# Optimization experiments

Hardware: AMD Instinct MI355X
Metric: run time of the kernel (lower is better)

## Reference

```python
import jax, jax.numpy as jnp
import numpy as np

B, S, DIN, DIM = 4, 4096, 256, 256
GAMMA = 0.9865


def setup_inputs() -> dict:
    key = jax.random.key(0)
    ks = jax.random.split(key, 9)
    inp = {
        'xq': jax.random.normal(ks[0], (B, S, DIN), dtype=jnp.float32),
        'xk': jax.random.normal(ks[1], (B, S, DIN), dtype=jnp.float32),
        'xv': jax.random.normal(ks[2], (B, S, DIN), dtype=jnp.float32),
        'Wq': jax.random.normal(ks[3], (DIN, DIM), dtype=jnp.float32) * 0.05,
        'bq': jnp.zeros((DIM,), dtype=jnp.float32),
        'Wk': jax.random.normal(ks[4], (DIN, DIM), dtype=jnp.float32) * 0.05,
        'bk': jnp.zeros((DIM,), dtype=jnp.float32),
        'Wv': jax.random.normal(ks[5], (DIN, DIM), dtype=jnp.float32) * 0.05,
        'bv': jnp.zeros((DIM,), dtype=jnp.float32),
    }
    return inp


def _decay_matrix(s, gamma):
    # D[i, j] = gamma^(i-j) if i >= j else 0
    idx = jnp.arange(s)
    diff = idx[:, None] - idx[None, :]
    D = jnp.where(diff >= 0,
                  jnp.power(jnp.float32(gamma), diff.astype(jnp.float32)),
                  jnp.float32(0.0))
    return D


def reference(xq, xk, xv, Wq, bq, Wk, bk, Wv, bv):
    Q = xq @ Wq + bq  # [B,S,D]
    K = xk @ Wk + bk  # [B,S,D]
    V = xv @ Wv + bv  # [B,S,D]
    d = Q.shape[-1]
    # scores[b,i,j] = Q[b,i] . K[b,j] / sqrt(d)
    x = jnp.einsum('bid,bjd->bij', Q, K) / jnp.sqrt(jnp.float32(d))
    D = _decay_matrix(S, GAMMA)
    # Faithful to TF broadcasting: divides along the LAST axis (per-column by
    # sqrt of that index's row-sum): D[i,j] /= sqrt(sum_k D[j,k])
    D = D / jnp.sqrt(jnp.sum(D, axis=-1))
    x = x * D  # broadcast [B,S,S] * [S,S]
    # _norm_3 per batch element with TF broadcasting: x[b,i,j] /= max(|sum_k x[b,j,k]|, 1)
    denom = jnp.maximum(jnp.abs(jnp.sum(x, axis=-1)), 1.0)  # [B,S]
    x = x / denom[:, None, :]
    return x @ V  # [B,S,D]
```

## Files before the change

### kernel.cpp

```cpp
#include <hip/hip_runtime.h>
#include <math.h>

#define BB 4
#define SS 4096
#define DD 256
#define LL 256
#define NCH 16
#define GAMMA 0.9865f
#define LOG2G (-0.019609034f)
#define INV1MG 74.07407407f
#define SLAB 1032
#define SLABB 520

typedef __attribute__((ext_vector_type(8))) short short8;
typedef __attribute__((ext_vector_type(4))) float f32x4;
typedef unsigned short u16;
typedef unsigned int u32;

__device__ __forceinline__ u16 f2bf(float f) {
  union { float f; unsigned u; } v; v.f = f;
  unsigned r = v.u + 0x7FFFu + ((v.u >> 16) & 1u);
  return (u16)(r >> 16);
}
__device__ __forceinline__ float bf2f(u16 h) {
  union { unsigned u; float f; } v; v.u = ((unsigned)h) << 16; return v.f;
}

__device__ __forceinline__ void gll16(const u16* g, u16* l) {
  __builtin_amdgcn_global_load_lds(
      (const __attribute__((address_space(1))) u32*)g,
      (__attribute__((address_space(3))) u32*)l, 16, 0, 0);
}
__device__ __forceinline__ void stage8kp(const u16* g, u16* l, int lane) {
#pragma unroll
  for (int i = 0; i < 8; ++i)
    gll16(g + i * 512 + lane * 8, l + (i >> 1) * SLAB + (i & 1) * 512);
}
__device__ __forceinline__ void stageB64(const u16* g, u16* l, int lane) {
#pragma unroll
  for (int i = 0; i < 4; ++i)
    gll16(g + i * 1024 + lane * 8, l + i * SLABB);
}
__device__ __forceinline__ void stageAB(
    const u16* AhP, const u16* AlP, const u16* BhP, const u16* BlP, int ks,
    u16* Ab, u16* Bb, int wave, int lane)
{
  if (wave == 0) stage8kp(AhP + ks * 4096, Ab, lane);
  if (wave == 1) stage8kp(AlP + ks * 4096, Ab + 4 * SLAB, lane);
  if (wave == 2) stageB64(BhP + ks * 4096, Bb, lane);
  if (wave == 3) stageB64(BlP + ks * 4096, Bb + 4 * SLABB, lane);
}

__device__ __forceinline__ void mfma_step_slab(
    const u16* Ah, const u16* Al, const u16* Bh, const u16* Bl,
    int wm0, int wn0, int fm, int fq, f32x4 acc[4][4])
{
  const int ka = fq * SLAB;
  short8 ah[4], al[4];
#pragma unroll
  for (int i = 0; i < 4; ++i) {
    ah[i] = *(const short8*)&Ah[ka + (wm0 + i * 16 + fm) * 8];
    al[i] = *(const short8*)&Al[ka + (wm0 + i * 16 + fm) * 8];
  }
#pragma unroll
  for (int j = 0; j < 4; ++j) {
    short8 bh = *(const short8*)&Bh[ka + (wn0 + j * 16 + fm) * 8];
    short8 bl = *(const short8*)&Bl[ka + (wn0 + j * 16 + fm) * 8];
#pragma unroll
    for (int i = 0; i < 4; ++i) {
      acc[i][j] = __builtin_amdgcn_mfma_f32_16x16x32_bf16(al[i], bh, acc[i][j], 0, 0, 0);
      acc[i][j] = __builtin_amdgcn_mfma_f32_16x16x32_bf16(ah[i], bl, acc[i][j], 0, 0, 0);
      acc[i][j] = __builtin_amdgcn_mfma_f32_16x16x32_bf16(ah[i], bh, acc[i][j], 0, 0, 0);
    }
  }
}

__device__ __forceinline__ void mfma_step_ab(
    const u16* Ah, const u16* Al, const u16* Bh, const u16* Bl,
    int wm0, int wn0, int fm, int fq, f32x4 acc[4][2])
{
  const int ka = fq * SLAB, kb = fq * SLABB;
  short8 ah[4], al[4];
#pragma unroll
  for (int i = 0; i < 4; ++i) {
    ah[i] = *(const short8*)&Ah[ka + (wm0 + i * 16 + fm) * 8];
    al[i] = *(const short8*)&Al[ka + (wm0 + i * 16 + fm) * 8];
  }
#pragma unroll
  for (int j = 0; j < 2; ++j) {
    short8 bh = *(const short8*)&Bh[kb + (wn0 + j * 16 + fm) * 8];
    short8 bl = *(const short8*)&Bl[kb + (wn0 + j * 16 + fm) * 8];
#pragma unroll
    for (int i = 0; i < 4; ++i) {
      acc[i][j] = __builtin_amdgcn_mfma_f32_16x16x32_bf16(al[i], bh, acc[i][j], 0, 0, 0);
      acc[i][j] = __builtin_amdgcn_mfma_f32_16x16x32_bf16(ah[i], bl, acc[i][j], 0, 0, 0);
      acc[i][j] = __builtin_amdgcn_mfma_f32_16x16x32_bf16(ah[i], bh, acc[i][j], 0, 0, 0);
    }
  }
}

__device__ __forceinline__ void bounce_write(
    float* fb, const f32x4 acc[4][4], int wm0, int wn0, int fm, int fq, int p)
{
  if (wn0 == p * 64) {
#pragma unroll
    for (int i = 0; i < 4; ++i)
#pragma unroll
      for (int j = 0; j < 4; ++j)
#pragma unroll
        for (int r = 0; r < 4; ++r)
          fb[(wm0 + i * 16 + fq * 4 + r) * 65 + j * 16 + fm] = acc[i][j][r];
  }
}

__global__ __launch_bounds__(256) void init_pack_kernel(
    const float* __restrict__ Wq, const float* __restrict__ Wk, const float* __restrict__ Wv,
    u16* __restrict__ Wth, u16* __restrict__ Wtl,
    float* __restrict__ rsP, float* __restrict__ lVec)
{
  const int which = blockIdx.x;
  const int it = blockIdx.y;
  const int t = threadIdx.x;
  if (which == 0) {
    *(float4*)&rsP[(size_t)(it * 256 + t) * 4] = (float4){0.f, 0.f, 0.f, 0.f};
  } else if (which == 1) {
    *(float4*)&lVec[(size_t)(it * 256 + t) * 4] = (float4){0.f, 0.f, 0.f, 0.f};
  }
  const float* W = which == 0 ? Wq : (which == 1 ? Wk : Wv);
  for (int pn = 0; pn < 2; ++pn) {
    int pos = it * 256 + t;
    int k8 = pos >> 7, r = pos & 127;
    u16 hs[8], ls[8];
#pragma unroll
    for (int u = 0; u < 8; ++u) {
      float x = W[(size_t)(k8 * 8 + u) * DD + pn * 128 + r];
      u16 h = f2bf(x); hs[u] = h; ls[u] = f2bf(x - bf2f(h));
    }
    size_t o = ((size_t)((which * 2 + pn) * 32 + k8)) * 1024 + (size_t)r * 8;
    *(short8*)&Wth[o] = *(short8*)hs;
    *(short8*)&Wtl[o] = *(short8*)ls;
  }
}

__device__ __forceinline__ void loadX(float xs[2][8], const float* XP, int ks,
                                      int arow, int ak8) {
#pragma unroll
  for (int t = 0; t < 2; ++t) {
    const float* src = XP + (size_t)(t * 64 + arow) * DD + ks * 32 + ak8 * 8;
    *(float4*)&xs[t][0] = *(const float4*)src;
    *(float4*)&xs[t][4] = *(const float4*)(src + 4);
  }
}
__device__ __forceinline__ void writeAsplit(u16* Ab, const float xs[2][8],
                                            int arow, int ak8) {
#pragma unroll
  for (int t = 0; t < 2; ++t) {
    int row = t * 64 + arow;
    u16 hs[8], ls[8];
#pragma unroll
    for (int u = 0; u < 8; ++u) {
      u16 h = f2bf(xs[t][u]); hs[u] = h; ls[u] = f2bf(xs[t][u] - bf2f(h));
    }
    *(short8*)&Ab[ak8 * SLAB + row * 8] = *(short8*)hs;
    *(short8*)&Ab[4 * SLAB + ak8 * SLAB + row * 8] = *(short8*)ls;
  }
}

__global__ __launch_bounds__(256, 2) void proj_kernel(
    const float* __restrict__ xq, const float* __restrict__ xk, const float* __restrict__ xv,
    const u16* __restrict__ Wth, const u16* __restrict__ Wtl,
    const float* __restrict__ bq, const float* __restrict__ bk_, const float* __restrict__ bv,
    u16* __restrict__ Qh, u16* __restrict__ Ql,
    u16* __restrict__ Kh, u16* __restrict__ Kl,
    u16* __restrict__ KTh, u16* __restrict__ KTl, float* __restrict__ VT32,
    float* __restrict__ lVec)
{
  const int which = blockIdx.z;
  const float* bias = which == 0 ? bq : (which == 1 ? bk_ : bv);
  const int m0 = blockIdx.x * 128;
  const int pn = blockIdx.y;
  __shared__ u16 SM[2 * 16 * SLAB];
  __shared__ float rsc[128];
  __shared__ float wlut[128];
  __shared__ float kacc[64];
  float* fb = (float*)SM;
  const int tid = threadIdx.x, lane = tid & 63, wave = tid >> 6;
  const int wm0 = (wave >> 1) * 64, wn0 = (wave & 1) * 64;
  const int fm = lane & 15, fq = lane >> 4;
  if (which == 1) {
    if (tid < 128) {
      int sb = (m0 & (SS - 1)) + tid;
      rsc[tid] = rsqrtf((1.0f - exp2f((float)(sb + 1) * LOG2G)) * INV1MG);
      wlut[tid] = exp2f((float)(255 - ((m0 & (LL - 1)) + tid)) * LOG2G);
    }
    if (tid < 64) kacc[tid] = 0.f;
  }
  const float* XP = (which == 0 ? xq : (which == 1 ? xk : xv)) + (size_t)m0 * DD;
  const u16* WhP = Wth + (size_t)((which * 2 + pn) * 32) * 1024;
  const u16* WlP = Wtl + (size_t)((which * 2 + pn) * 32) * 1024;
  const int arow = tid >> 2, ak8 = tid & 3;
  f32x4 acc[4][4];
#pragma unroll
  for (int i = 0; i < 4; ++i)
#pragma unroll
    for (int j = 0; j < 4; ++j) acc[i][j] = (f32x4){0.f, 0.f, 0.f, 0.f};
  float xs[2][8];
  loadX(xs, XP, 0, arow, ak8);
  writeAsplit(SM, xs, arow, ak8);
  if (wave == 2) stage8kp(WhP, SM + 8 * SLAB, lane);
  if (wave == 3) stage8kp(WlP, SM + 12 * SLAB, lane);
  int cur = 0;
  for (int ks = 0; ks < 8; ++ks) {
    __syncthreads();
    u16* Bc = cur ? SM + 16 * SLAB : SM;
    u16* Bn = cur ? SM : SM + 16 * SLAB;
    if (ks < 7) {
      loadX(xs, XP, ks + 1, arow, ak8);
      if (wave == 2) stage8kp(WhP + (ks + 1) * 4096, Bn + 8 * SLAB, lane);
      if (wave == 3) stage8kp(WlP + (ks + 1) * 4096, Bn + 12 * SLAB, lane);
    }
    mfma_step_slab(Bc, Bc + 4 * SLAB, Bc + 8 * SLAB, Bc + 12 * SLAB,
                   wm0, wn0, fm, fq, acc);
    if (ks < 7) writeAsplit(Bn, xs, arow, ak8);
    cur ^= 1;
  }
  const int b = m0 >> 12, sbb = m0 & (SS - 1);
  for (int p = 0; p < 2; ++p) {
    __syncthreads();
    bounce_write(fb, acc, wm0, wn0, fm, fq, p);
    __syncthreads();
    if (which == 0) {
#pragma unroll
      for (int it = 0; it < 4; ++it) {
        int unit = it * 256 + tid;
        int k8l = unit >> 7, row = unit & 127;
        int gcol0 = pn * 128 + p * 64 + k8l * 8;
        u16 hs[8], ls[8];
#pragma unroll
        for (int u = 0; u < 8; ++u) {
          float v = (fb[row * 65 + k8l * 8 + u] + bias[gcol0 + u]) * (1.f / 16.f);
          u16 h = f2bf(v); hs[u] = h; ls[u] = f2bf(v - bf2f(h));
        }
        size_t o = (size_t)(m0 >> 7) * 32768 + (size_t)(pn * 16 + p * 8 + k8l) * 1024 + row * 8;
        *(short8*)&Qh[o] = *(short8*)hs;
        *(short8*)&Ql[o] = *(short8*)ls;
      }
    } else if (which == 1) {
#pragma unroll
      for (int it = 0; it < 4; ++it) {
        int unit = it * 256 + tid;
        int k8l = unit >> 7, row = unit & 127;
        int gcol0 = pn * 128 + p * 64 + k8l * 8;
        u16 hs[8], ls[8];
#pragma unroll
        for (int u = 0; u < 8; ++u) {
          float v = (fb[row * 65 + k8l * 8 + u] + bias[gcol0 + u]) * rsc[row];
          u16 h = f2bf(v); hs[u] = h; ls[u] = f2bf(v - bf2f(h));
        }
        size_t o = (size_t)(m0 >> 7) * 32768 + (size_t)(pn * 16 + p * 8 + k8l) * 1024 + row * 8;
        *(short8*)&Kh[o] = *(short8*)hs;
        *(short8*)&Kl[o] = *(short8*)ls;
      }
      float kpart = 0.f;
#pragma unroll
      for (int it = 0; it < 4; ++it) {
        int unit = it * 256 + tid;
        int dl = unit & 63, s8l = unit >> 6;
        int gcolg = pn * 128 + p * 64 + dl;
        float bs = bias[gcolg];
        u16 hs[8], ls[8];
#pragma unroll
        for (int u = 0; u < 8; ++u) {
          int row = s8l * 8 + u;
          float v = (fb[row * 65 + dl] + bs) * rsc[row];
          kpart = fmaf(v, wlut[row], kpart);
          u16 h = f2bf(v); hs[u] = h; ls[u] = f2bf(v - bf2f(h));
        }
        int sb0 = sbb + s8l * 8;
        size_t o = ((size_t)(b * 2 + (gcolg >> 7)) * 512 + (sb0 >> 3)) * 1024 + (size_t)(gcolg & 127) * 8;
        *(short8*)&KTh[o] = *(short8*)hs;
        *(short8*)&KTl[o] = *(short8*)ls;
      }
      atomicAdd(&kacc[tid & 63], kpart);
      __syncthreads();
      if (tid < 64) {
        int c = sbb >> 8;
        atomicAdd(&lVec[(size_t)(b * NCH + c) * DD + pn * 128 + p * 64 + tid], kacc[tid]);
        kacc[tid] = 0.f;
      }
    } else {
#pragma unroll
      for (int it = 0; it < 4; ++it) {
        int unit = it * 256 + tid;
        int dl = unit & 63, s8l = unit >> 6;
        int gcolg = pn * 128 + p * 64 + dl;
        float bs = bias[gcolg];
        float vv[8];
#pragma unroll
        for (int u = 0; u < 8; ++u) vv[u] = fb[(s8l * 8 + u) * 65 + dl] + bs;
        float* dst = &VT32[(size_t)b * DD * SS + (size_t)gcolg * SS + sbb + s8l * 8];
        *(float4*)dst = (float4){vv[0], vv[1], vv[2], vv[3]};
        *(float4*)(dst + 4) = (float4){vv[4], vv[5], vv[6], vv[7]};
      }
    }
  }
}

__global__ __launch_bounds__(256, 3) void scores_kernel(
    const u16* __restrict__ Qh, const u16* __restrict__ Ql,
    const u16* __restrict__ Kh, const u16* __restrict__ Kl,
    const float* __restrict__ lVec, u16* __restrict__ Sgh, u16* __restrict__ Sgl,
    float* __restrict__ rsP)
{
  const int chunk = blockIdx.x, b = chunk >> 4, c = chunk & 15;
  const int y = blockIdx.y;
  const int m0 = (y < 2) ? 0 : 128;
  const int jn0 = (y < 2) ? y * 64 : (y - 2) * 64;
  __shared__ u16 SA[2 * 8 * SLAB];
  __shared__ u16 SB[2 * 8 * SLABB];
  __shared__ float cv[256], lut[256], rowAcc[128], qd2[2][128];
  float* fb = (float*)SA;
  const int tid = threadIdx.x, lane = tid & 63, wave = tid >> 6;
  const int wm0 = (wave >> 1) * 64, wn0 = (wave & 1) * 32;
  const int fm = lane & 15, fq = lane >> 4;
  if (jn0 == 0) {
    const float gL = exp2f((float)LL * LOG2G);
    float s = 0.f;
    for (int cp = 0; cp < c; ++cp)
      s = fmaf(gL, s, lVec[(size_t)(b * NCH + cp) * DD + tid]);
    cv[tid] = s;
  }
  lut[tid] = exp2f((float)tid * LOG2G);
  if (tid < 128) rowAcc[tid] = 0.f;
  const int growA = b * SS + c * LL + m0;
  const int growB = b * SS + c * LL + jn0;
  const u16* QhP = Qh + (size_t)(growA >> 7) * 32768;
  const u16* QlP = Ql + (size_t)(growA >> 7) * 32768;
  const u16* KhP = Kh + (size_t)(growB >> 7) * 32768 + (size_t)(growB & 127) * 8;
  const u16* KlP = Kl + (size_t)(growB >> 7) * 32768 + (size_t)(growB & 127) * 8;
  f32x4 acc[4][2];
#pragma unroll
  for (int i = 0; i < 4; ++i)
#pragma unroll
    for (int j = 0; j < 2; ++j) acc[i][j] = (f32x4){0.f, 0.f, 0.f, 0.f};
  float qdreg = 0.f;
  const int qrow = tid & 127, qk8b = tid >> 7;
  stageAB(QhP, QlP, KhP, KlP, 0, SA, SB, wave, lane);
  int cur = 0;
  for (int ks = 0; ks < 8; ++ks) {
    __syncthreads();
    u16* Ac = cur ? SA + 8 * SLAB : SA;
    u16* Bc = cur ? SB + 8 * SLABB : SB;
    u16* An = cur ? SA : SA + 8 * SLAB;
    u16* Bn = cur ? SB : SB + 8 * SLABB;
    if (ks < 7) stageAB(QhP, QlP, KhP, KlP, ks + 1, An, Bn, wave, lane);
    mfma_step_ab(Ac, Ac + 4 * SLAB, Bc, Bc + 4 * SLABB, wm0, wn0, fm, fq, acc);
    if (jn0 == 0) {
#pragma unroll
      for (int h2 = 0; h2 < 2; ++h2) {
        int k8l = qk8b + 2 * h2;
        const u16* ahp = &Ac[k8l * SLAB + qrow * 8];
        const u16* alp = &Ac[4 * SLAB + k8l * SLAB + qrow * 8];
#pragma unroll
        for (int u = 0; u < 8; ++u)
          qdreg = fmaf(bf2f(ahp[u]) + bf2f(alp[u]), cv[ks * 32 + k8l * 8 + u], qdreg);
      }
    }
    cur ^= 1;
  }
  qd2[qk8b][qrow] = qdreg;
  const int ps = chunk * 2 + (m0 >> 7);
  for (int rh = 0; rh < 2; ++rh) {
    __syncthreads();
    if (wm0 == rh * 64) {
#pragma unroll
      for (int i = 0; i < 4; ++i)
#pragma unroll
        for (int j = 0; j < 2; ++j)
#pragma unroll
          for (int r = 0; r < 4; ++r)
            fb[(i * 16 + fq * 4 + r) * 65 + wn0 + j * 16 + fm] = acc[i][j][r];
    }
    __syncthreads();
#pragma unroll
    for (int it = 0; it < 2; ++it) {
      int unit = it * 256 + tid;
      int k8l = unit >> 6, rowl = unit & 63;
      int il = m0 + rh * 64 + rowl;
      int jlb = jn0 + k8l * 8;
      float part = 0.f;
      u16 hs[8], ls[8];
#pragma unroll
      for (int u = 0; u < 8; ++u) {
        int jl = jlb + u;
        float v = (jl <= il) ? fb[rowl * 65 + k8l * 8 + u] * lut[il - jl] : 0.f;
        part += v;
        u16 h = f2bf(v); hs[u] = h; ls[u] = f2bf(v - bf2f(h));
      }
      atomicAdd(&rowAcc[rh * 64 + rowl], part);
      size_t o = (size_t)(ps * 32 + (jn0 >> 3) + k8l) * 1024 + (size_t)(rh * 64 + rowl) * 8;
      *(short8*)&Sgh[o] = *(short8*)hs;
      *(short8*)&Sgl[o] = *(short8*)ls;
    }
  }
  __syncthreads();
  if (tid < 128) {
    float rs = rowAcc[tid];
    if (jn0 == 0)
      rs += exp2f((float)(m0 + tid + 1) * LOG2G) * (qd2[0][tid] + qd2[1][tid]);
    atomicAdd(&rsP[(size_t)b * SS + c * LL + m0 + tid], rs);
  }
}

__global__ __launch_bounds__(256, 3) void lmat_kernel(
    const float* __restrict__ VT32, const float* __restrict__ rsP,
    const u16* __restrict__ KTh, const u16* __restrict__ KTl,
    float* __restrict__ lMatT)
{
  const int chunk = blockIdx.x, b = chunk >> 4, c = chunk & 15;
  const int ty = blockIdx.y;
  const int m0 = (ty >> 2) * 128, n0 = (ty & 3) * 64;
  __shared__ u16 SA[2 * 8 * SLAB];
  __shared__ u16 SB[2 * 8 * SLABB];
  __shared__ float swl[256];
  const int tid = threadIdx.x, lane = tid & 63, wave = tid >> 6;
  const int wm0 = (wave >> 1) * 64, wn0 = (wave & 1) * 32;
  const int fm = lane & 15, fq = lane >> 4;
  swl[tid] = exp2f((float)(255 - tid) * LOG2G) /
             fmaxf(fabsf(rsP[(size_t)b * SS + c * LL + tid]), 1.0f);
  const float* AP = VT32 + (size_t)b * DD * SS + (size_t)m0 * SS + c * LL;
  const u16* BhP = KTh + ((size_t)(b * 2 + (n0 >> 7)) * 512 + c * 32) * 1024 + (size_t)(n0 & 127) * 8;
  const u16* BlP = KTl + ((size_t)(b * 2 + (n0 >> 7)) * 512 + c * 32) * 1024 + (size_t)(n0 & 127) * 8;
  const int arow = tid >> 1;
  f32x4 acc[4][2];
#pragma unroll
  for (int i = 0; i < 4; ++i)
#pragma unroll
    for (int j = 0; j < 2; ++j) acc[i][j] = (f32x4){0.f, 0.f, 0.f, 0.f};
  float as[2][8];
#pragma unroll
  for (int t = 0; t < 2; ++t) {
    int ak8 = (tid & 1) * 2 + t;
    const float* src = AP + (size_t)arow * SS + ak8 * 8;
    *(float4*)&as[t][0] = *(const float4*)src;
    *(float4*)&as[t][4] = *(const float4*)(src + 4);
  }
  __syncthreads();
#pragma unroll
  for (int t = 0; t < 2; ++t) {
    int ak8 = (tid & 1) * 2 + t;
    u16 hs[8], ls[8];
#pragma unroll
    for (int u = 0; u < 8; ++u) {
      float v = as[t][u] * swl[ak8 * 8 + u];
      u16 h = f2bf(v); hs[u] = h; ls[u] = f2bf(v - bf2f(h));
    }
    *(short8*)&SA[ak8 * SLAB + arow * 8] = *(short8*)hs;
    *(short8*)&SA[4 * SLAB + ak8 * SLAB + arow * 8] = *(short8*)ls;
  }
  if (wave == 2) stageB64(BhP, SB, lane);
  if (wave == 3) stageB64(BlP, SB + 4 * SLABB, lane);
  int cur = 0;
  for (int ks = 0; ks < 8; ++ks) {
    __syncthreads();
    u16* Ac = cur ? SA + 8 * SLAB : SA;
    u16* Bc = cur ? SB + 8 * SLABB : SB;
    u16* An = cur ? SA : SA + 8 * SLAB;
    u16* Bn = cur ? SB : SB + 8 * SLABB;
    if (ks < 7) {
#pragma unroll
      for (int t = 0; t < 2; ++t) {
        int ak8 = (tid & 1) * 2 + t;
        const float* src = AP + (size_t)arow * SS + (ks + 1) * 32 + ak8 * 8;
        *(float4*)&as[t][0] = *(const float4*)src;
        *(float4*)&as[t][4] = *(const float4*)(src + 4);
      }
      if (wave == 2) stageB64(BhP + (ks + 1) * 4096, Bn, lane);
      if (wave == 3) stageB64(BlP + (ks + 1) * 4096, Bn + 4 * SLABB, lane);
    }
    mfma_step_ab(Ac, Ac + 4 * SLAB, Bc, Bc + 4 * SLABB, wm0, wn0, fm, fq, acc);
    if (ks < 7) {
#pragma unroll
      for (int t = 0; t < 2; ++t) {
        int ak8 = (tid & 1) * 2 + t;
        u16 hs[8], ls[8];
#pragma unroll
        for (int u = 0; u < 8; ++u) {
          float v = as[t][u] * swl[(ks + 1) * 32 + ak8 * 8 + u];
          u16 h = f2bf(v); hs[u] = h; ls[u] = f2bf(v - bf2f(h));
        }
        *(short8*)&An[ak8 * SLAB + arow * 8] = *(short8*)hs;
        *(short8*)&An[4 * SLAB + ak8 * SLAB + arow * 8] = *(short8*)ls;
      }
    }
    cur ^= 1;
  }
#pragma unroll
  for (int i = 0; i < 4; ++i)
#pragma unroll
    for (int j = 0; j < 2; ++j)
#pragma unroll
      for (int r = 0; r < 4; ++r) {
        int e = m0 + wm0 + i * 16 + fq * 4 + r;
        int d = n0 + wn0 + j * 16 + fm;
        lMatT[(size_t)chunk * 65536 + (size_t)e * 256 + d] = acc[i][j][r];
      }
}

__global__ __launch_bounds__(256) void combine_mat_kernel(
    const float* __restrict__ lMatT, u16* __restrict__ cMh, u16* __restrict__ cMl)
{
  const int t = blockIdx.x * 256 + threadIdx.x;
  const int b = t >> 13, rem = t & 8191;
  const int k8 = rem >> 8, e = rem & 255;
  const float gL = powf(GAMMA, (float)LL);
  float s[8] = {0.f, 0.f, 0.f, 0.f, 0.f, 0.f, 0.f, 0.f};
  for (int ch = 0; ch < 16; ++ch) {
    size_t ro = (size_t)(b * 16 + ch) * 65536 + (size_t)e * 256 + k8 * 8;
    float4 a0 = *(const float4*)&lMatT[ro];
    float4 a1 = *(const float4*)&lMatT[ro + 4];
    float vals[8] = {a0.x, a0.y, a0.z, a0.w, a1.x, a1.y, a1.z, a1.w};
    u16 hh[8], ll[8];
#pragma unroll
    for (int u = 0; u < 8; ++u) {
      u16 h = f2bf(s[u]); hh[u] = h; ll[u] = f2bf(s[u] - bf2f(h));
    }
    size_t wo = ((size_t)(((b * 16 + ch) * 2 + (e >> 7)) * 32 + k8)) * 1024 + (size_t)(e & 127) * 8;
    *(short8*)&cMh[wo] = *(short8*)hh;
    *(short8*)&cMl[wo] = *(short8*)ll;
#pragma unroll
    for (int u = 0; u < 8; ++u) s[u] = gL * s[u] + vals[u];
  }
}

__global__ __launch_bounds__(256, 3) void out_kernel(
    const u16* __restrict__ Qh, const u16* __restrict__ Ql,
    const u16* __restrict__ cMh, const u16* __restrict__ cMl,
    const u16* __restrict__ Sgh, const u16* __restrict__ Sgl,
    const float* __restrict__ VT32, const float* __restrict__ rsP,
    float* __restrict__ out)
{
  const int chunk = blockIdx.x, b = chunk >> 4, c = chunk & 15;
  const int ty = blockIdx.y;
  const int m0 = (ty >> 2) * 128, n0 = (ty & 3) * 64;
  __shared__ u16 SA[2 * 8 * SLAB];
  __shared__ u16 SB[2 * 8 * SLABB];
  __shared__ float olut[128];
  __shared__ float sdn[256];
  const int tid = threadIdx.x, lane = tid & 63, wave = tid >> 6;
  const int wm0 = (wave >> 1) * 64, wn0 = (wave & 1) * 32;
  const int fm = lane & 15, fq = lane >> 4;
  if (tid < 128) olut[tid] = exp2f((float)(m0 + tid + 1) * LOG2G);
  sdn[tid] = 1.0f / fmaxf(fabsf(rsP[(size_t)b * SS + c * LL + tid]), 1.0f);
  f32x4 acc[4][2];
#pragma unroll
  for (int i = 0; i < 4; ++i)
#pragma unroll
    for (int j = 0; j < 2; ++j) acc[i][j] = (f32x4){0.f, 0.f, 0.f, 0.f};
  int cur = 0;
  {
    const u16* AhP = Qh + (size_t)(b * 32 + c * 2 + (m0 >> 7)) * 32768;
    const u16* AlP = Ql + (size_t)(b * 32 + c * 2 + (m0 >> 7)) * 32768;
    const u16* BhP = cMh + (size_t)(chunk * 2 + (n0 >> 7)) * 32768 + (size_t)(n0 & 127) * 8;
    const u16* BlP = cMl + (size_t)(chunk * 2 + (n0 >> 7)) * 32768 + (size_t)(n0 & 127) * 8;
    stageAB(AhP, AlP, BhP, BlP, 0, SA, SB, wave, lane);
    for (int ks = 0; ks < 8; ++ks) {
      __syncthreads();
      u16* Ac = cur ? SA + 8 * SLAB : SA;
      u16* Bc = cur ? SB + 8 * SLABB : SB;
      u16* An = cur ? SA : SA + 8 * SLAB;
      u16* Bn = cur ? SB : SB + 8 * SLABB;
      if (ks < 7) stageAB(AhP, AlP, BhP, BlP, ks + 1, An, Bn, wave, lane);
      mfma_step_ab(Ac, Ac + 4 * SLAB, Bc, Bc + 4 * SLABB, wm0, wn0, fm, fq, acc);
      cur ^= 1;
    }
  }
  {
    const u16* AhP = Sgh + (size_t)(chunk * 2 + (m0 >> 7)) * 32768;
    const u16* AlP = Sgl + (size_t)(chunk * 2 + (m0 >> 7)) * 32768;
    const float* BP = VT32 + (size_t)b * DD * SS + (size_t)n0 * SS + c * LL;
    const int ber = tid >> 2, bk8 = tid & 3;
    const int nks = (m0 >> 5) + 4;
    float bs[8];
    {
      u16* Ac = cur ? SA + 8 * SLAB : SA;
      u16* Bc = cur ? SB + 8 * SLABB : SB;
      if (wave == 0) stage8kp(AhP, Ac, lane);
      if (wave == 1) stage8kp(AlP, Ac + 4 * SLAB, lane);
      const float* src = BP + (size_t)ber * SS + bk8 * 8;
      *(float4*)&bs[0] = *(const float4*)src;
      *(float4*)&bs[4] = *(const float4*)(src + 4);
#pragma unroll
      for (int i = 0; i < 4; ++i)
#pragma unroll
        for (int r = 0; r < 4; ++r) {
          int rl = wm0 + i * 16 + fq * 4 + r;
          float sc = olut[rl];
#pragma unroll
          for (int j = 0; j < 2; ++j) acc[i][j][r] *= sc;
        }
      u16 hs[8], ls[8];
#pragma unroll
      for (int u = 0; u < 8; ++u) {
        float v = bs[u] * sdn[bk8 * 8 + u];
        u16 h = f2bf(v); hs[u] = h; ls[u] = f2bf(v - bf2f(h));
      }
      *(short8*)&Bc[bk8 * SLABB + ber * 8] = *(short8*)hs;
      *(short8*)&Bc[4 * SLABB + bk8 * SLABB + ber * 8] = *(short8*)ls;
    }
    for (int ks = 0; ks < nks; ++ks) {
      __syncthreads();
      u16* Ac = cur ? SA + 8 * SLAB : SA;
      u16* Bc = cur ? SB + 8 * SLABB : SB;
      u16* An = cur ? SA : SA + 8 * SLAB;
      u16* Bn = cur ? SB : SB + 8 * SLABB;
      if (ks + 1 < nks) {
        if (wave == 0) stage8kp(AhP + (ks + 1) * 4096, An, lane);
        if (wave == 1) stage8kp(AlP + (ks + 1) * 4096, An + 4 * SLAB, lane);
        const float* src = BP + (size_t)ber * SS + (ks + 1) * 32 + bk8 * 8;
        *(float4*)&bs[0] = *(const float4*)src;
        *(float4*)&bs[4] = *(const float4*)(src + 4);
      }
      mfma_step_ab(Ac, Ac + 4 * SLAB, Bc, Bc + 4 * SLABB, wm0, wn0, fm, fq, acc);
      if (ks + 1 < nks) {
        u16 hs[8], ls[8];
#pragma unroll
        for (int u = 0; u < 8; ++u) {
          float v = bs[u] * sdn[(ks + 1) * 32 + bk8 * 8 + u];
          u16 h = f2bf(v); hs[u] = h; ls[u] = f2bf(v - bf2f(h));
        }
        *(short8*)&Bn[bk8 * SLABB + ber * 8] = *(short8*)hs;
        *(short8*)&Bn[4 * SLABB + bk8 * SLABB + ber * 8] = *(short8*)ls;
      }
      cur ^= 1;
    }
  }
#pragma unroll
  for (int i = 0; i < 4; ++i)
#pragma unroll
    for (int j = 0; j < 2; ++j)
#pragma unroll
      for (int r = 0; r < 4; ++r) {
        int il = m0 + wm0 + i * 16 + fq * 4 + r;
        int e = n0 + wn0 + j * 16 + fm;
        out[(size_t)(b * SS + c * LL + il) * DD + e] = acc[i][j][r];
      }
}

extern "C" void kernel_launch(void* const* d_in, const int* in_sizes, int n_in,
                              void* d_out, int out_size, void* d_ws, size_t ws_size,
                              hipStream_t stream) {
  const float* xq = (const float*)d_in[0];
  const float* xk = (const float*)d_in[1];
  const float* xv = (const float*)d_in[2];
  const float* Wq = (const float*)d_in[3];
  const float* bq = (const float*)d_in[4];
  const float* Wk = (const float*)d_in[5];
  const float* bk = (const float*)d_in[6];
  const float* Wv = (const float*)d_in[7];
  const float* bv = (const float*)d_in[8];
  float* out = (float*)d_out;

  char* p = (char*)d_ws;
  const size_t H16 = (size_t)BB * SS * DD * 2;
  u16* Qh   = (u16*)(p + 0 * H16);  u16* Ql   = (u16*)(p + 1 * H16);
  u16* Kh   = (u16*)(p + 2 * H16);  u16* Kl   = (u16*)(p + 3 * H16);
  u16* KTh  = (u16*)(p + 4 * H16);  u16* KTl  = (u16*)(p + 5 * H16);
  u16* Sgh  = (u16*)(p + 10 * H16); u16* Sgl  = (u16*)(p + 11 * H16);
  u16* cMh  = (u16*)(p + 12 * H16); u16* cMl  = (u16*)(p + 13 * H16);
  float* lMatT = (float*)(p + 14 * H16);
  float* VT32  = (float*)(p + 16 * H16);
  u16* Wth = (u16*)(p + 18 * H16);
  u16* Wtl = (u16*)(p + 18 * H16 + 3 * DD * DD * 2);
  float* rsP  = (float*)(p + 18 * H16 + 6 * DD * DD * 2);
  float* lVec = rsP + (size_t)BB * SS;

  init_pack_kernel<<<dim3(3, 16), 256, 0, stream>>>(Wq, Wk, Wv, Wth, Wtl, rsP, lVec);
  proj_kernel<<<dim3(BB * SS / 128, 2, 3), 256, 0, stream>>>(
      xq, xk, xv, Wth, Wtl, bq, bk, bv, Qh, Ql, Kh, Kl, KTh, KTl, VT32, lVec);
  scores_kernel<<<dim3(BB * NCH, 6), 256, 0, stream>>>(
      Qh, Ql, Kh, Kl, lVec, Sgh, Sgl, rsP);
  lmat_kernel<<<dim3(BB * NCH, 8), 256, 0, stream>>>(VT32, rsP, KTh, KTl, lMatT);
  combine_mat_kernel<<<128, 256, 0, stream>>>(lMatT, cMh, cMl);
  out_kernel<<<dim3(BB * NCH, 8), 256, 0, stream>>>(
      Qh, Ql, cMh, cMl, Sgh, Sgl, VT32, rsP, out);
}
```

Baseline: 206.2 us.

## Relax barrier waits, swizzle LDS staging, reorder async loads, trim shared memory

Several loop barriers become a custom wait on lgkmcnt followed by s_barrier, so global loads in flight are no longer drained at every iteration. Async weight and K staging is issued before the register loads so more memory traffic overlaps. The k8 slot each thread writes is rotated by row and the slab padding changes, both aimed at fewer LDS bank conflicts. In the scores kernel, rowAcc and qd2 now alias the SB buffer to save LDS, and Q reads are vectorised into short8 loads. The relaxed barrier risks reading data that global_load_lds has not finished writing if the compiler does not add its own vmcnt wait.

```diff
diff --git a/kernel.cpp b/kernel.cpp
--- a/kernel.cpp
+++ b/kernel.cpp
@@ -9,13 +9,15 @@
 #define GAMMA 0.9865f
 #define LOG2G (-0.019609034f)
 #define INV1MG 74.07407407f
-#define SLAB 1032
-#define SLABB 520
+#define SLAB 1040
+#define SLABB 528
 
 typedef __attribute__((ext_vector_type(8))) short short8;
 typedef __attribute__((ext_vector_type(4))) float f32x4;
 typedef unsigned short u16;
 typedef unsigned int u32;
+
+#define BARLG() asm volatile("s_waitcnt lgkmcnt(0)\n\ts_barrier" ::: "memory")
 
 __device__ __forceinline__ u16 f2bf(float f) {
   union { float f; unsigned u; } v; v.f = f;
@@ -198,26 +200,26 @@
   const float* XP = (which == 0 ? xq : (which == 1 ? xk : xv)) + (size_t)m0 * DD;
   const u16* WhP = Wth + (size_t)((which * 2 + pn) * 32) * 1024;
   const u16* WlP = Wtl + (size_t)((which * 2 + pn) * 32) * 1024;
-  const int arow = tid >> 2, ak8 = tid & 3;
+  const int arow = tid >> 2, ak8 = (tid + (tid >> 2)) & 3;
   f32x4 acc[4][4];
 #pragma unroll
   for (int i = 0; i < 4; ++i)
 #pragma unroll
     for (int j = 0; j < 4; ++j) acc[i][j] = (f32x4){0.f, 0.f, 0.f, 0.f};
   float xs[2][8];
+  if (wave == 2) stage8kp(WhP, SM + 8 * SLAB, lane);
+  if (wave == 3) stage8kp(WlP, SM + 12 * SLAB, lane);
   loadX(xs, XP, 0, arow, ak8);
   writeAsplit(SM, xs, arow, ak8);
-  if (wave == 2) stage8kp(WhP, SM + 8 * SLAB, lane);
-  if (wave == 3) stage8kp(WlP, SM + 12 * SLAB, lane);
   int cur = 0;
   for (int ks = 0; ks < 8; ++ks) {
-    __syncthreads();
+    BARLG();
     u16* Bc = cur ? SM + 16 * SLAB : SM;
     u16* Bn = cur ? SM : SM + 16 * SLAB;
     if (ks < 7) {
-      loadX(xs, XP, ks + 1, arow, ak8);
       if (wave == 2) stage8kp(WhP + (ks + 1) * 4096, Bn + 8 * SLAB, lane);
       if (wave == 3) stage8kp(WlP + (ks + 1) * 4096, Bn + 12 * SLAB, lane);
+      loadX(xs, XP, ks + 1, arow, ak8);
     }
     mfma_step_slab(Bc, Bc + 4 * SLAB, Bc + 8 * SLAB, Bc + 12 * SLAB,
                    wm0, wn0, fm, fq, acc);
@@ -318,7 +320,9 @@
   const int jn0 = (y < 2) ? y * 64 : (y - 2) * 64;
   __shared__ u16 SA[2 * 8 * SLAB];
   __shared__ u16 SB[2 * 8 * SLABB];
-  __shared__ float cv[256], lut[256], rowAcc[128], qd2[2][128];
+  __shared__ float cv[256], lut[256];
+  float* rowAcc = (float*)SB;
+  float* qd2 = (float*)SB + 128;
   float* fb = (float*)SA;
   const int tid = threadIdx.x, lane = tid & 63, wave = tid >> 6;
   const int wm0 = (wave >> 1) * 64, wn0 = (wave & 1) * 32;
@@ -331,7 +335,6 @@
     cv[tid] = s;
   }
   lut[tid] = exp2f((float)tid * LOG2G);
-  if (tid < 128) rowAcc[tid] = 0.f;
   const int growA = b * SS + c * LL + m0;
   const int growB = b * SS + c * LL + jn0;
   const u16* QhP = Qh + (size_t)(growA >> 7) * 32768;
@@ -359,19 +362,23 @@
 #pragma unroll
       for (int h2 = 0; h2 < 2; ++h2) {
         int k8l = qk8b + 2 * h2;
-        const u16* ahp = &Ac[k8l * SLAB + qrow * 8];
-        const u16* alp = &Ac[4 * SLAB + k8l * SLAB + qrow * 8];
+        short8 hv = *(const short8*)&Ac[k8l * SLAB + qrow * 8];
+        short8 lv = *(const short8*)&Ac[4 * SLAB + k8l * SLAB + qrow * 8];
 #pragma unroll
         for (int u = 0; u < 8; ++u)
-          qdreg = fmaf(bf2f(ahp[u]) + bf2f(alp[u]), cv[ks * 32 + k8l * 8 + u], qdreg);
+          qdreg = fmaf(bf2f((u16)hv[u]) + bf2f((u16)lv[u]),
+                       cv[ks * 32 + k8l * 8 + u], qdreg);
       }
     }
     cur ^= 1;
   }
-  qd2[qk8b][qrow] = qdreg;
   const int ps = chunk * 2 + (m0 >> 7);
   for (int rh = 0; rh < 2; ++rh) {
     __syncthreads();
+    if (rh == 0) {
+      if (tid < 128) rowAcc[tid] = 0.f;
+      qd2[qk8b * 128 + qrow] = qdreg;
+    }
     if (wm0 == rh * 64) {
 #pragma unroll
       for (int i = 0; i < 4; ++i)
@@ -407,7 +414,7 @@
   if (tid < 128) {
     float rs = rowAcc[tid];
     if (jn0 == 0)
-      rs += exp2f((float)(m0 + tid + 1) * LOG2G) * (qd2[0][tid] + qd2[1][tid]);
+      rs += exp2f((float)(m0 + tid + 1) * LOG2G) * (qd2[tid] + qd2[128 + tid]);
     atomicAdd(&rsP[(size_t)b * SS + c * LL + m0 + tid], rs);
   }
 }
@@ -438,9 +445,11 @@
 #pragma unroll
     for (int j = 0; j < 2; ++j) acc[i][j] = (f32x4){0.f, 0.f, 0.f, 0.f};
   float as[2][8];
+  if (wave == 2) stageB64(BhP, SB, lane);
+  if (wave == 3) stageB64(BlP, SB + 4 * SLABB, lane);
 #pragma unroll
   for (int t = 0; t < 2; ++t) {
-    int ak8 = (tid & 1) * 2 + t;
+    int ak8 = ((tid & 1) * 2 + t + arow) & 3;
     const float* src = AP + (size_t)arow * SS + ak8 * 8;
     *(float4*)&as[t][0] = *(const float4*)src;
     *(float4*)&as[t][4] = *(const float4*)(src + 4);
@@ -448,7 +457,7 @@
   __syncthreads();
 #pragma unroll
   for (int t = 0; t < 2; ++t) {
-    int ak8 = (tid & 1) * 2 + t;
+    int ak8 = ((tid & 1) * 2 + t + arow) & 3;
     u16 hs[8], ls[8];
 #pragma unroll
     for (int u = 0; u < 8; ++u) {
@@ -458,31 +467,29 @@
     *(short8*)&SA[ak8 * SLAB + arow * 8] = *(short8*)hs;
     *(short8*)&SA[4 * SLAB + ak8 * SLAB + arow * 8] = *(short8*)ls;
   }
-  if (wave == 2) stageB64(BhP, SB, lane);
-  if (wave == 3) stageB64(BlP, SB + 4 * SLABB, lane);
   int cur = 0;
   for (int ks = 0; ks < 8; ++ks) {
-    __syncthreads();
+    BARLG();
     u16* Ac = cur ? SA + 8 * SLAB : SA;
     u16* Bc = cur ? SB + 8 * SLABB : SB;
     u16* An = cur ? SA : SA + 8 * SLAB;
     u16* Bn = cur ? SB : SB + 8 * SLABB;
     if (ks < 7) {
+      if (wave == 2) stageB64(BhP + (ks + 1) * 4096, Bn, lane);
+      if (wave == 3) stageB64(BlP + (ks + 1) * 4096, Bn + 4 * SLABB, lane);
 #pragma unroll
       for (int t = 0; t < 2; ++t) {
-        int ak8 = (tid & 1) * 2 + t;
+        int ak8 = ((tid & 1) * 2 + t + arow) & 3;
         const float* src = AP + (size_t)arow * SS + (ks + 1) * 32 + ak8 * 8;
         *(float4*)&as[t][0] = *(const float4*)src;
         *(float4*)&as[t][4] = *(const float4*)(src + 4);
       }
-      if (wave == 2) stageB64(BhP + (ks + 1) * 4096, Bn, lane);
-      if (wave == 3) stageB64(BlP + (ks + 1) * 4096, Bn + 4 * SLABB, lane);
     }
     mfma_step_ab(Ac, Ac + 4 * SLAB, Bc, Bc + 4 * SLABB, wm0, wn0, fm, fq, acc);
     if (ks < 7) {
 #pragma unroll
       for (int t = 0; t < 2; ++t) {
-        int ak8 = (tid & 1) * 2 + t;
+        int ak8 = ((tid & 1) * 2 + t + arow) & 3;
         u16 hs[8], ls[8];
 #pragma unroll
         for (int u = 0; u < 8; ++u) {
@@ -579,7 +586,7 @@
     const u16* AhP = Sgh + (size_t)(chunk * 2 + (m0 >> 7)) * 32768;
     const u16* AlP = Sgl + (size_t)(chunk * 2 + (m0 >> 7)) * 32768;
     const float* BP = VT32 + (size_t)b * DD * SS + (size_t)n0 * SS + c * LL;
-    const int ber = tid >> 2, bk8 = tid & 3;
+    const int ber = tid >> 2, bk8 = (tid + (tid >> 2)) & 3;
     const int nks = (m0 >> 5) + 4;
     float bs[8];
     {
@@ -609,7 +616,7 @@
       *(short8*)&Bc[4 * SLABB + bk8 * SLABB + ber * 8] = *(short8*)ls;
     }
     for (int ks = 0; ks < nks; ++ks) {
-      __syncthreads();
+      BARLG();
       u16* Ac = cur ? SA + 8 * SLAB : SA;
       u16* Bc = cur ? SB + 8 * SLABB : SB;
       u16* An = cur ? SA : SA + 8 * SLAB;
```

Result: slower. 212.1 us (+2.9%).

## Load projection weights straight into registers instead of staging through LDS

Applied to the files above, without the earlier changes.

In the projection kernel, the weight hi/lo bf16 fragments are now read from global memory directly into registers for each k-step. They are no longer copied into shared memory by two dedicated waves. This halves the LDS footprint, which allows the launch bound to rise from two to three blocks per CU, and it removes the LDS round trip for B. The cost is more global/L2 traffic, since every wave re-reads its own weight slices. The next step's weight loads are also issued after the MFMAs, so their latency may be exposed.

```diff
diff --git a/kernel.cpp b/kernel.cpp
--- a/kernel.cpp
+++ b/kernel.cpp
@@ -51,9 +51,9 @@
   if (wave == 3) stageB64(BlP + ks * 4096, Bb + 4 * SLABB, lane);
 }
 
-__device__ __forceinline__ void mfma_step_slab(
-    const u16* Ah, const u16* Al, const u16* Bh, const u16* Bl,
-    int wm0, int wn0, int fm, int fq, f32x4 acc[4][4])
+__device__ __forceinline__ void mfma_step_regB(
+    const u16* Ah, const u16* Al, const short8 bh[4], const short8 bl[4],
+    int wm0, int fm, int fq, f32x4 acc[4][4])
 {
   const int ka = fq * SLAB;
   short8 ah[4], al[4];
@@ -63,15 +63,24 @@
     al[i] = *(const short8*)&Al[ka + (wm0 + i * 16 + fm) * 8];
   }
 #pragma unroll
+  for (int j = 0; j < 4; ++j)
+#pragma unroll
+    for (int i = 0; i < 4; ++i) {
+      acc[i][j] = __builtin_amdgcn_mfma_f32_16x16x32_bf16(al[i], bh[j], acc[i][j], 0, 0, 0);
+      acc[i][j] = __builtin_amdgcn_mfma_f32_16x16x32_bf16(ah[i], bl[j], acc[i][j], 0, 0, 0);
+      acc[i][j] = __builtin_amdgcn_mfma_f32_16x16x32_bf16(ah[i], bh[j], acc[i][j], 0, 0, 0);
+    }
+}
+
+__device__ __forceinline__ void loadBW(short8 bh[4], short8 bl[4],
+    const u16* WhP, const u16* WlP, int ks, int wn0, int fm, int fq)
+{
+  const int base = ks * 4096 + fq * 1024;
+#pragma unroll
   for (int j = 0; j < 4; ++j) {
-    short8 bh = *(const short8*)&Bh[ka + (wn0 + j * 16 + fm) * 8];
-    short8 bl = *(const short8*)&Bl[ka + (wn0 + j * 16 + fm) * 8];
-#pragma unroll
-    for (int i = 0; i < 4; ++i) {
-      acc[i][j] = __builtin_amdgcn_mfma_f32_16x16x32_bf16(al[i], bh, acc[i][j], 0, 0, 0);
-      acc[i][j] = __builtin_amdgcn_mfma_f32_16x16x32_bf16(ah[i], bl, acc[i][j], 0, 0, 0);
-      acc[i][j] = __builtin_amdgcn_mfma_f32_16x16x32_bf16(ah[i], bh, acc[i][j], 0, 0, 0);
-    }
+    int o = base + (wn0 + j * 16 + fm) * 8;
+    bh[j] = *(const short8*)&WhP[o];
+    bl[j] = *(const short8*)&WlP[o];
   }
 }
 
@@ -166,7 +175,7 @@
   }
 }
 
-__global__ __launch_bounds__(256, 2) void proj_kernel(
+__global__ __launch_bounds__(256, 3) void proj_kernel(
     const float* __restrict__ xq, const float* __restrict__ xk, const float* __restrict__ xv,
     const u16* __restrict__ Wth, const u16* __restrict__ Wtl,
     const float* __restrict__ bq, const float* __restrict__ bk_, const float* __restrict__ bv,
@@ -179,7 +188,7 @@
   const float* bias = which == 0 ? bq : (which == 1 ? bk_ : bv);
   const int m0 = blockIdx.x * 128;
   const int pn = blockIdx.y;
-  __shared__ u16 SM[2 * 16 * SLAB];
+  __shared__ u16 SM[16 * SLAB + 128];
   __shared__ float rsc[128];
   __shared__ float wlut[128];
   __shared__ float kacc[64];
@@ -205,23 +214,21 @@
 #pragma unroll
     for (int j = 0; j < 4; ++j) acc[i][j] = (f32x4){0.f, 0.f, 0.f, 0.f};
   float xs[2][8];
+  short8 bh[4], bl[4];
+  loadBW(bh, bl, WhP, WlP, 0, wn0, fm, fq);
   loadX(xs, XP, 0, arow, ak8);
   writeAsplit(SM, xs, arow, ak8);
-  if (wave == 2) stage8kp(WhP, SM + 8 * SLAB, lane);
-  if (wave == 3) stage8kp(WlP, SM + 12 * SLAB, lane);
   int cur = 0;
   for (int ks = 0; ks < 8; ++ks) {
     __syncthreads();
-    u16* Bc = cur ? SM + 16 * SLAB : SM;
-    u16* Bn = cur ? SM : SM + 16 * SLAB;
+    u16* Ac = SM + cur * 8 * SLAB;
+    u16* An = SM + (cur ^ 1) * 8 * SLAB;
+    if (ks < 7) loadX(xs, XP, ks + 1, arow, ak8);
+    mfma_step_regB(Ac, Ac + 4 * SLAB, bh, bl, wm0, fm, fq, acc);
     if (ks < 7) {
-      loadX(xs, XP, ks + 1, arow, ak8);
-      if (wave == 2) stage8kp(WhP + (ks + 1) * 4096, Bn + 8 * SLAB, lane);
-      if (wave == 3) stage8kp(WlP + (ks + 1) * 4096, Bn + 12 * SLAB, lane);
-    }
-    mfma_step_slab(Bc, Bc + 4 * SLAB, Bc + 8 * SLAB, Bc + 12 * SLAB,
-                   wm0, wn0, fm, fq, acc);
-    if (ks < 7) writeAsplit(Bn, xs, arow, ak8);
+      loadBW(bh, bl, WhP, WlP, ks + 1, wn0, fm, fq);
+      writeAsplit(An, xs, arow, ak8);
+    }
     cur ^= 1;
   }
   const int b = m0 >> 12, sbb = m0 & (SS - 1);
```

After: 202.1 us. 1.02x faster.
